# Optimization experiments

Hardware: AMD Instinct MI355X
Metric: run time of the kernel (lower is better)

The kernel has to match this reference:

```python
import jax, jax.numpy as jnp
import numpy as np


def setup_inputs() -> dict:
    key = jax.random.key(0)
    ks = jax.random.split(key, 5)
    B, S, D, H, DK = 2, 2048, 1024, 16, 64
    scale = 1.0 / np.sqrt(D)
    return {
        "x": jax.random.normal(ks[0], (B, S, D), dtype=jnp.float32),
        "Wq": jax.random.normal(ks[1], (H, D, DK), dtype=jnp.float32) * scale,
        "Wk": jax.random.normal(ks[2], (H, D, DK), dtype=jnp.float32) * scale,
        "Wv": jax.random.normal(ks[3], (H, D, DK), dtype=jnp.float32) * scale,
        "Wo": jax.random.normal(ks[4], (D, D), dtype=jnp.float32) * scale,
    }


def reference(x, Wq, Wk, Wv, Wo):
    # x: (B, S, D); Wq/Wk/Wv: (H, D, d_k); Wo: (D, D) torch-Linear convention (y = c @ Wo.T)
    B, S, D = x.shape
    H, _, dk = Wq.shape
    Q = jnp.einsum('bsd,hdk->bhsk', x, Wq)  # (B,H,S,dk)
    K = jnp.einsum('bsd,hdk->bhsk', x, Wk)
    V = jnp.einsum('bsd,hdk->bhsk', x, Wv)
    scores = jnp.einsum('bhqk,bhsk->bhqs', Q, K) / jnp.sqrt(jnp.float32(dk))  # (B,H,S,S)
    causal = jnp.tril(jnp.ones((S, S), dtype=bool))
    scores = jnp.where(causal[None, None, :, :], scores, -jnp.inf)
    weights = jax.nn.softmax(scores, axis=-1)
    out = jnp.einsum('bhqs,bhsk->bhqk', weights, V)  # (B,H,S,dk)
    concat = out.transpose(0, 2, 1, 3).reshape(B, S, H * dk)  # heads concatenated h-major
    return concat @ Wo.T
```

## Files before the change

### kernel.cpp

```cpp
#include <hip/hip_runtime.h>

typedef unsigned short u16;
typedef unsigned int u32;
typedef __bf16 bf16x8 __attribute__((ext_vector_type(8)));
typedef float f32x4 __attribute__((ext_vector_type(4)));
typedef u16 u16x8 __attribute__((ext_vector_type(8)));
typedef u16 u16x4 __attribute__((ext_vector_type(4)));
typedef u32 u32x4 __attribute__((ext_vector_type(4)));

#define NH 16
#define DKK 64
#define SQ 2048
#define DD 1024

#define AS1 __attribute__((address_space(1)))
#define AS3 __attribute__((address_space(3)))

#define QSCALE 0.1803368925f

#define WAIT4 do { asm volatile("s_waitcnt vmcnt(4)" ::: "memory"); \
                   __builtin_amdgcn_sched_barrier(0); } while (0)
#define WAIT3 do { asm volatile("s_waitcnt vmcnt(3)" ::: "memory"); \
                   __builtin_amdgcn_sched_barrier(0); } while (0)
#define WAIT0 do { asm volatile("s_waitcnt vmcnt(0)" ::: "memory"); \
                   __builtin_amdgcn_sched_barrier(0); } while (0)
#define LWAIT0 do { asm volatile("s_waitcnt lgkmcnt(0)" ::: "memory"); \
                    __builtin_amdgcn_sched_barrier(0); } while (0)
#define BAR   __builtin_amdgcn_s_barrier()

__device__ inline u16 f2bf(float f) {
  union { float f; u32 u; } v; v.f = f;
  u32 u = v.u;
  u += 0x7FFFu + ((u >> 16) & 1u);
  return (u16)(u >> 16);
}

__device__ __forceinline__ u32 cvtpk(float lo, float hi) {
  u32 r;
  asm("v_cvt_pk_bf16_f32 %0, %1, %2" : "=v"(r) : "v"(lo), "v"(hi));
  return r;
}

__device__ inline u16x8 cvt8(const float* p) {
  float4 a = *(const float4*)p;
  float4 b = *(const float4*)(p + 4);
  u16x8 v;
  v[0] = f2bf(a.x); v[1] = f2bf(a.y); v[2] = f2bf(a.z); v[3] = f2bf(a.w);
  v[4] = f2bf(b.x); v[5] = f2bf(b.y); v[6] = f2bf(b.z); v[7] = f2bf(b.w);
  return v;
}

__device__ __forceinline__ void gload16(const u16* g, u16* l) {
  __builtin_amdgcn_global_load_lds((const AS1 u32*)(const void*)g,
                                   (AS3 u32*)(void*)l, 16, 0, 0);
}

__global__ __launch_bounds__(256) void prep_kernel(const float* __restrict__ x,
                                                   u16* __restrict__ xb,
                                                   const float* __restrict__ Wo,
                                                   u16* __restrict__ Wob,
                                                   const float* __restrict__ Wq,
                                                   const float* __restrict__ Wk,
                                                   const float* __restrict__ Wv,
                                                   u16* __restrict__ WT) {
  __shared__ u16 sm[64][72];
  int bid = blockIdx.x;
  int tid = threadIdx.x;
  if (bid < 2560) {
    const float* src; u16* dst; size_t base;
    if (bid < 2048) { src = x;  dst = xb;  base = (size_t)bid * 2048; }
    else            { src = Wo; dst = Wob; base = (size_t)(bid - 2048) * 2048; }
    size_t off = base + (size_t)tid * 8;
    *(u16x8*)&dst[off] = cvt8(&src[off]);
    return;
  }
  int wid = bid - 2560;
  int t = wid >> 8;
  int rem = wid & 255;
  int h = rem >> 4;
  int d0 = (rem & 15) * 64;
  const float* src = (t == 0) ? Wq : (t == 1) ? Wk : Wv;
  for (int j = 0; j < 2; ++j) {
    int idx = tid + j * 256;
    int r = idx >> 3;
    int c0 = (idx & 7) * 8;
    *(u16x8*)&sm[r][c0] = cvt8(&src[(h * DD + d0 + r) * DKK + c0]);
  }
  __syncthreads();
  for (int j = 0; j < 2; ++j) {
    int idx = tid + j * 256;
    int r2 = idx >> 3;
    int c0 = (idx & 7) * 8;
    u16x8 vv;
    for (int i = 0; i < 8; ++i) vv[i] = sm[c0 + i][r2];
    int n = t * 1024 + h * 64 + r2;
    *(u16x8*)&WT[n * DD + d0 + c0] = vv;
  }
}

__global__ __launch_bounds__(256) void gemm128(const u16* __restrict__ A,
                                               const u16* __restrict__ Bm,
                                               u16* __restrict__ o0,
                                               u16* __restrict__ o1,
                                               u16* __restrict__ o2) {
  __shared__ u16 As[2][128 * 32];
  __shared__ u16 Bs[2][128 * 32];
  const int K = 1024;
  int m0 = blockIdx.x * 128;
  int n0 = blockIdx.y * 128;
  int tid = threadIdx.x;
  int w = tid >> 6, l = tid & 63;
  int lg = l >> 4, lr = l & 15;
  int wr = w >> 1, wc = w & 1;

  int srow = w * 32 + (l >> 2);
  int sg = (l & 3) ^ ((l >> 3) & 3);
  const u16* gA = A + (size_t)(m0 + srow) * K + sg * 8;
  const u16* gB = Bm + (size_t)(n0 + srow) * K + sg * 8;
  int gsw = (lr >> 1) & 3;

  #define GSTAGE(buf, k0)                              \
    do {                                               \
      gload16(gA + (k0), &As[buf][w * 1024]);          \
      gload16(gA + (k0) + 16 * K, &As[buf][w * 1024 + 512]); \
      gload16(gB + (k0), &Bs[buf][w * 1024]);          \
      gload16(gB + (k0) + 16 * K, &Bs[buf][w * 1024 + 512]); \
    } while (0)

  f32x4 acc[4][4] = {};
  GSTAGE(0, 0);
  for (int kt = 0; kt < 32; ++kt) {
    int buf = kt & 1;
    if (kt < 31) { GSTAGE(buf ^ 1, (kt + 1) * 32); WAIT4; }
    else         { WAIT0; }
    BAR;
    bf16x8 a[4], b[4];
    #pragma unroll
    for (int m = 0; m < 4; ++m)
      a[m] = *(const bf16x8*)&As[buf][(wr * 64 + m * 16 + lr) * 32 + ((lg ^ gsw) * 8)];
    #pragma unroll
    for (int n = 0; n < 4; ++n)
      b[n] = *(const bf16x8*)&Bs[buf][(wc * 64 + n * 16 + lr) * 32 + ((lg ^ gsw) * 8)];
    #pragma unroll
    for (int m = 0; m < 4; ++m)
      #pragma unroll
      for (int n = 0; n < 4; ++n)
        acc[m][n] = __builtin_amdgcn_mfma_f32_16x16x32_bf16(a[m], b[n], acc[m][n], 0, 0, 0);
    BAR;
  }
  #undef GSTAGE

  {
    int t = n0 >> 10;
    int h = (((n0 & 1023) + wc * 64) >> 6);
    int bq = m0 >> 11;
    int sbase = (m0 & 2047) + wr * 64 + lg * 4;
    if (t < 2) {
      float sc = (t == 0) ? QSCALE : 1.0f;
      u16* o = (t == 0) ? o0 : o1;
      u16* op = o + (size_t)(bq * NH + h) * SQ * DKK;
      #pragma unroll
      for (int m = 0; m < 4; ++m)
        #pragma unroll
        for (int n = 0; n < 4; ++n)
          #pragma unroll
          for (int rr = 0; rr < 4; ++rr)
            op[(size_t)(sbase + m * 16 + rr) * DKK + n * 16 + lr] = f2bf(acc[m][n][rr] * sc);
    } else {
      u16* op = o2 + (size_t)(bq * NH + h) * DKK * SQ;
      int Sb = (m0 & 2047) + wr * 64;
      #pragma unroll
      for (int m = 0; m < 4; ++m)
        #pragma unroll
        for (int n = 0; n < 4; ++n) {
          u16x4 vv;
          #pragma unroll
          for (int rr = 0; rr < 4; ++rr) vv[rr] = f2bf(acc[m][n][rr]);
          *(u16x4*)&op[(size_t)(n * 16 + lr) * SQ + Sb + (m >> 1) * 32 + lg * 8 + (m & 1) * 4] = vv;
        }
    }
  }
}

__global__ __launch_bounds__(256) void gemm_wo(const u16* __restrict__ A,
                                               const u16* __restrict__ Bm,
                                               float* __restrict__ of) {
  __shared__ u16 As[2][128 * 32];
  __shared__ u16 Bs[2][64 * 32];
  const int K = 1024;
  int m0 = blockIdx.x * 128;
  int n0 = blockIdx.y * 64;
  int tid = threadIdx.x;
  int w = tid >> 6, l = tid & 63;
  int lg = l >> 4, lr = l & 15;
  int wr = w >> 1, wc = w & 1;

  int sg = (l & 3) ^ ((l >> 3) & 3);
  const u16* gA = A + (size_t)(m0 + w * 32 + (l >> 2)) * K + sg * 8;
  const u16* gB = Bm + (size_t)(n0 + w * 16 + (l >> 2)) * K + sg * 8;
  int gsw = (lr >> 1) & 3;

  #define WSTAGE(buf, k0)                              \
    do {                                               \
      gload16(gA + (k0), &As[buf][w * 1024]);          \
      gload16(gA + (k0) + 16 * K, &As[buf][w * 1024 + 512]); \
      gload16(gB + (k0), &Bs[buf][w * 512]);           \
    } while (0)

  f32x4 acc[4][2] = {};
  WSTAGE(0, 0);
  for (int kt = 0; kt < 32; ++kt) {
    int buf = kt & 1;
    if (kt < 31) { WSTAGE(buf ^ 1, (kt + 1) * 32); WAIT3; }
    else         { WAIT0; }
    BAR;
    bf16x8 a[4], b[2];
    #pragma unroll
    for (int m = 0; m < 4; ++m)
      a[m] = *(const bf16x8*)&As[buf][(wr * 64 + m * 16 + lr) * 32 + ((lg ^ gsw) * 8)];
    #pragma unroll
    for (int n = 0; n < 2; ++n)
      b[n] = *(const bf16x8*)&Bs[buf][(wc * 32 + n * 16 + lr) * 32 + ((lg ^ gsw) * 8)];
    #pragma unroll
    for (int m = 0; m < 4; ++m)
      #pragma unroll
      for (int n = 0; n < 2; ++n)
        acc[m][n] = __builtin_amdgcn_mfma_f32_16x16x32_bf16(a[m], b[n], acc[m][n], 0, 0, 0);
    BAR;
  }
  #undef WSTAGE

  int mbase = m0 + wr * 64 + lg * 4;
  int nbase = n0 + wc * 32 + lr;
  #pragma unroll
  for (int m = 0; m < 4; ++m)
    #pragma unroll
    for (int n = 0; n < 2; ++n)
      #pragma unroll
      for (int rr = 0; rr < 4; ++rr)
        of[(size_t)(mbase + m * 16 + rr) * 1024 + nbase + n * 16] = acc[m][n][rr];
}

__global__ __launch_bounds__(256) void attn_kernel(const u16* __restrict__ Q,
                                                   const u16* __restrict__ Kg,
                                                   const u16* __restrict__ Vt,
                                                   u16* __restrict__ Cc) {
  __shared__ u16 Ks[2][64 * 64];
  __shared__ u16 Vs[2][64 * 64];
  int bh = blockIdx.x;
  int y = blockIdx.y;
  int a = y & 7, bsel = y >> 3;
  int s = (bsel == 0) ? 2 * a : (bsel == 1) ? 2 * a + 1
        : (bsel == 2) ? 30 - 2 * a : 31 - 2 * a;
  int tid = threadIdx.x;
  int w = tid >> 6, l = tid & 63;
  int lg = l >> 4, lr = l & 15;
  const u16* Qp = Q + (size_t)bh * SQ * DKK;
  const u16* Kp = Kg + (size_t)bh * SQ * DKK;
  const u16* Vp = Vt + (size_t)bh * DKK * SQ;
  int b = bh >> 4, h = bh & 15;

  int lrow8 = l >> 3;
  int swz = (l & 7) ^ lrow8;
  int r7 = lr & 7;
  const u16* kSrc0 = Kp + (size_t)(w * 16 + lrow8) * DKK + swz * 8;
  const u16* kSrc1 = Kp + (size_t)(w * 16 + 8 + lrow8) * DKK + swz * 8;
  const u16* vSrc0 = Vp + (size_t)(w * 16 + lrow8) * SQ + swz * 8;
  const u16* vSrc1 = Vp + (size_t)(w * 16 + 8 + lrow8) * SQ + swz * 8;

  #define STAGE(buf, j0)                                                  \
    do {                                                                  \
      gload16(kSrc0 + (size_t)(j0) * DKK, &Ks[buf][(w * 16) * 64]);       \
      gload16(kSrc1 + (size_t)(j0) * DKK, &Ks[buf][(w * 16 + 8) * 64]);   \
      gload16(vSrc0 + (j0), &Vs[buf][(w * 16) * 64]);                     \
      gload16(vSrc1 + (j0), &Vs[buf][(w * 16 + 8) * 64]);                 \
    } while (0)

  int qrow = s * 64 + w * 16 + lr;
  bf16x8 qf0 = *(const bf16x8*)&Qp[(size_t)qrow * DKK + lg * 8];
  bf16x8 qf1 = *(const bf16x8*)&Qp[(size_t)qrow * DKK + 32 + lg * 8];

  STAGE(0, 0);

  f32x4 o[4] = {};
  float lpart = 0.f, suPrev = 0.f;
  union { u16x8 u; bf16x8 v; } zz;
  #pragma unroll
  for (int i = 0; i < 8; ++i) zz.u[i] = 0;
  bf16x8 paPrev0 = zz.v, paPrev1 = zz.v;
  bf16x8 vPrev0[4], vPrev1[4];
  #pragma unroll
  for (int n = 0; n < 4; ++n) { vPrev0[n] = zz.v; vPrev1[n] = zz.v; }

  for (int jt = 0; jt <= s; ++jt) {
    int cur = jt & 1;
    if (jt < s) { STAGE(cur ^ 1, (jt + 1) * 64); WAIT4; }
    else        { WAIT0; }
    BAR;

    float p[16];
    __builtin_amdgcn_s_setprio(1);
    #pragma unroll
    for (int c = 0; c < 4; ++c) {
      int R = c * 16 + lr;
      const u16* kr = &Ks[cur][R * 64];
      bf16x8 k0 = *(const bf16x8*)&kr[(lg ^ r7) * 8];
      bf16x8 k1 = *(const bf16x8*)&kr[((4 + lg) ^ r7) * 8];
      f32x4 z = {};
      z = __builtin_amdgcn_mfma_f32_16x16x32_bf16(k0, qf0, z, 0, 0, 0);
      z = __builtin_amdgcn_mfma_f32_16x16x32_bf16(k1, qf1, z, 0, 0, 0);
      #pragma unroll
      for (int rr = 0; rr < 4; ++rr) p[c * 4 + rr] = z[rr];
    }
    #pragma unroll
    for (int n = 0; n < 4; ++n) {
      o[n] = __builtin_amdgcn_mfma_f32_16x16x32_bf16(paPrev0, vPrev0[n], o[n], 0, 0, 0);
      o[n] = __builtin_amdgcn_mfma_f32_16x16x32_bf16(paPrev1, vPrev1[n], o[n], 0, 0, 0);
    }
    __builtin_amdgcn_s_setprio(0);
    lpart += suPrev;
    #pragma unroll
    for (int n = 0; n < 4; ++n) {
      int R2 = n * 16 + lr;
      vPrev0[n] = *(const bf16x8*)&Vs[cur][R2 * 64 + ((lg ^ r7) * 8)];
      vPrev1[n] = *(const bf16x8*)&Vs[cur][R2 * 64 + (((4 + lg) ^ r7) * 8)];
    }
    if (jt == s) {
      int j0 = jt * 64;
      #pragma unroll
      for (int c = 0; c < 4; ++c)
        #pragma unroll
        for (int rr = 0; rr < 4; ++rr) {
          int kv = j0 + c * 16 + lg * 4 + rr;
          if (kv > qrow) p[c * 4 + rr] = -1e30f;
        }
    }
    float su = 0.f;
    #pragma unroll
    for (int i = 0; i < 16; ++i) { p[i] = exp2f(p[i]); su += p[i]; }
    suPrev = su;
    union { u32x4 w; bf16x8 v; } pk0, pk1;
    pk0.w[0] = cvtpk(p[0],  p[1]);
    pk0.w[1] = cvtpk(p[2],  p[3]);
    pk0.w[2] = cvtpk(p[4],  p[5]);
    pk0.w[3] = cvtpk(p[6],  p[7]);
    pk1.w[0] = cvtpk(p[8],  p[9]);
    pk1.w[1] = cvtpk(p[10], p[11]);
    pk1.w[2] = cvtpk(p[12], p[13]);
    pk1.w[3] = cvtpk(p[14], p[15]);
    paPrev0 = pk0.v;
    paPrev1 = pk1.v;
    LWAIT0;
    BAR;
  }

  #pragma unroll
  for (int n = 0; n < 4; ++n) {
    o[n] = __builtin_amdgcn_mfma_f32_16x16x32_bf16(paPrev0, vPrev0[n], o[n], 0, 0, 0);
    o[n] = __builtin_amdgcn_mfma_f32_16x16x32_bf16(paPrev1, vPrev1[n], o[n], 0, 0, 0);
  }
  lpart += suPrev;

  float lsum = lpart;
  lsum += __shfl_xor(lsum, 16, 64);
  lsum += __shfl_xor(lsum, 32, 64);
  float lrow[4];
  #pragma unroll
  for (int rr = 0; rr < 4; ++rr) lrow[rr] = __shfl(lsum, lg * 4 + rr, 64);
  int srow = s * 64 + w * 16 + lg * 4;
  #pragma unroll
  for (int n = 0; n < 4; ++n)
    #pragma unroll
    for (int rr = 0; rr < 4; ++rr) {
      float val = o[n][rr] / lrow[rr];
      Cc[((size_t)(b * SQ + srow + rr)) * DD + h * DKK + n * 16 + lr] = f2bf(val);
    }
  #undef STAGE
}

extern "C" void kernel_launch(void* const* d_in, const int* in_sizes, int n_in,
                              void* d_out, int out_size, void* d_ws, size_t ws_size,
                              hipStream_t stream) {
  (void)in_sizes; (void)n_in; (void)out_size; (void)ws_size;
  const float* x  = (const float*)d_in[0];
  const float* Wq = (const float*)d_in[1];
  const float* Wk = (const float*)d_in[2];
  const float* Wv = (const float*)d_in[3];
  const float* Wo = (const float*)d_in[4];
  float* out = (float*)d_out;
  u16* ws = (u16*)d_ws;
  u16* WT  = ws;
  u16* Qb  = WT + 3145728;
  u16* Kb  = Qb + 4194304;
  u16* Vb  = Kb + 4194304;
  u16* XC  = Vb + 4194304;
  u16* Wob = XC + 4194304;

  hipLaunchKernelGGL(prep_kernel, dim3(3328), dim3(256), 0, stream, x, XC, Wo, Wob, Wq, Wk, Wv, WT);
  hipLaunchKernelGGL(gemm128, dim3(32, 24), dim3(256), 0, stream, XC, WT, Qb, Kb, Vb);
  hipLaunchKernelGGL(attn_kernel, dim3(32, 32), dim3(256), 0, stream, Qb, Kb, Vb, XC);
  hipLaunchKernelGGL(gemm_wo, dim3(32, 16), dim3(256), 0, stream, XC, Wob, out);
}
```

Before: 106.7 us.

## Triple-buffer LDS staging in QKV GEMM and attention to drop a barrier

New measurement: 131.7 us. 1.23x slower.

```diff
diff --git a/kernel.cpp b/kernel.cpp
--- a/kernel.cpp
+++ b/kernel.cpp
@@ -103,8 +103,8 @@
                                                u16* __restrict__ o0,
                                                u16* __restrict__ o1,
                                                u16* __restrict__ o2) {
-  __shared__ u16 As[2][128 * 32];
-  __shared__ u16 Bs[2][128 * 32];
+  __shared__ u16 As[3][128 * 32];
+  __shared__ u16 Bs[3][128 * 32];
   const int K = 1024;
   int m0 = blockIdx.x * 128;
   int n0 = blockIdx.y * 128;
@@ -127,28 +127,34 @@
       gload16(gB + (k0) + 16 * K, &Bs[buf][w * 1024 + 512]); \
     } while (0)
 
+  #define GCOMP(BC)                                                            \
+    do {                                                                       \
+      bf16x8 a[4], b[4];                                                       \
+      _Pragma("unroll")                                                        \
+      for (int m = 0; m < 4; ++m)                                              \
+        a[m] = *(const bf16x8*)&As[BC][(wr * 64 + m * 16 + lr) * 32 + ((lg ^ gsw) * 8)]; \
+      _Pragma("unroll")                                                        \
+      for (int n = 0; n < 4; ++n)                                              \
+        b[n] = *(const bf16x8*)&Bs[BC][(wc * 64 + n * 16 + lr) * 32 + ((lg ^ gsw) * 8)]; \
+      _Pragma("unroll")                                                        \
+      for (int m = 0; m < 4; ++m)                                              \
+        _Pragma("unroll")                                                      \
+        for (int n = 0; n < 4; ++n)                                            \
+          acc[m][n] = __builtin_amdgcn_mfma_f32_16x16x32_bf16(a[m], b[n], acc[m][n], 0, 0, 0); \
+    } while (0)
+
   f32x4 acc[4][4] = {};
   GSTAGE(0, 0);
-  for (int kt = 0; kt < 32; ++kt) {
-    int buf = kt & 1;
-    if (kt < 31) { GSTAGE(buf ^ 1, (kt + 1) * 32); WAIT4; }
-    else         { WAIT0; }
-    BAR;
-    bf16x8 a[4], b[4];
-    #pragma unroll
-    for (int m = 0; m < 4; ++m)
-      a[m] = *(const bf16x8*)&As[buf][(wr * 64 + m * 16 + lr) * 32 + ((lg ^ gsw) * 8)];
-    #pragma unroll
-    for (int n = 0; n < 4; ++n)
-      b[n] = *(const bf16x8*)&Bs[buf][(wc * 64 + n * 16 + lr) * 32 + ((lg ^ gsw) * 8)];
-    #pragma unroll
-    for (int m = 0; m < 4; ++m)
-      #pragma unroll
-      for (int n = 0; n < 4; ++n)
-        acc[m][n] = __builtin_amdgcn_mfma_f32_16x16x32_bf16(a[m], b[n], acc[m][n], 0, 0, 0);
-    BAR;
-  }
+  GSTAGE(1, 32);
+  for (int kt = 0; kt < 30; kt += 3) {
+    WAIT4; BAR; GSTAGE(2, (kt + 2) * 32); GCOMP(0);
+    WAIT4; BAR; GSTAGE(0, (kt + 3) * 32); GCOMP(1);
+    WAIT4; BAR; GSTAGE(1, (kt + 4) * 32); GCOMP(2);
+  }
+  WAIT4; BAR; GCOMP(0);
+  WAIT0; BAR; GCOMP(1);
   #undef GSTAGE
+  #undef GCOMP
 
   {
     int t = n0 >> 10;
@@ -245,8 +251,8 @@
                                                    const u16* __restrict__ Kg,
                                                    const u16* __restrict__ Vt,
                                                    u16* __restrict__ Cc) {
-  __shared__ u16 Ks[2][64 * 64];
-  __shared__ u16 Vs[2][64 * 64];
+  __shared__ u16 Ks[3][64 * 64];
+  __shared__ u16 Vs[3][64 * 64];
   int bh = blockIdx.x;
   int y = blockIdx.y;
   int a = y & 7, bsel = y >> 3;
@@ -281,6 +287,7 @@
   bf16x8 qf1 = *(const bf16x8*)&Qp[(size_t)qrow * DKK + 32 + lg * 8];
 
   STAGE(0, 0);
+  if (s >= 1) STAGE(1, 64);
 
   f32x4 o[4] = {};
   float lpart = 0.f, suPrev = 0.f;
@@ -292,11 +299,14 @@
   #pragma unroll
   for (int n = 0; n < 4; ++n) { vPrev0[n] = zz.v; vPrev1[n] = zz.v; }
 
+  int cur = 0;
   for (int jt = 0; jt <= s; ++jt) {
-    int cur = jt & 1;
-    if (jt < s) { STAGE(cur ^ 1, (jt + 1) * 64); WAIT4; }
-    else        { WAIT0; }
+    if (jt < s) WAIT4; else WAIT0;
     BAR;
+    if (jt + 2 <= s) {
+      int bs = (cur == 0) ? 2 : cur - 1;
+      STAGE(bs, (jt + 2) * 64);
+    }
 
     float p[16];
     __builtin_amdgcn_s_setprio(1);
@@ -351,7 +361,7 @@
     paPrev0 = pk0.v;
     paPrev1 = pk1.v;
     LWAIT0;
-    BAR;
+    cur = (cur == 2) ? 0 : cur + 1;
   }
 
   #pragma unroll
```

## Split long causal attention rows across two blocks and combine partial sums

Applied to the files above, without the earlier changes.

Result: slower. 110.6 us (+3.7%).

```diff
diff --git a/kernel.cpp b/kernel.cpp
--- a/kernel.cpp
+++ b/kernel.cpp
@@ -28,11 +28,26 @@
                     __builtin_amdgcn_sched_barrier(0); } while (0)
 #define BAR   __builtin_amdgcn_s_barrier()
 
+__constant__ int TS[48]  = {15,31,31,30,14,13,28,11,  28,29,29,30,12,23,24,21,
+                            26,27,27,26,22,23,20,21,  24,25,25,18,16,19,19,22,
+                             6, 5, 4, 7,17,17,20,10,   0, 1, 2, 3,16,18, 8, 9};
+__constant__ int TT0[48] = { 0, 0,16, 0, 0, 0,15, 0,   0, 0,15,16, 0, 0,13, 0,
+                             0, 0,14,14, 0,12, 0,11,   0, 0,13, 0, 0, 0,10,12,
+                             0, 0, 0, 0, 0, 9,11, 0,   0, 0, 0, 0, 9,10, 0, 0};
+__constant__ int TNT[48] = {16,16,16,16,15,14,14,12,  15,15,15,15,13,12,12,11,
+                            14,14,14,13,12,12,11,11,  13,13,13,10, 9,10,10,11,
+                             7, 6, 5, 8, 9, 9,10,11,   1, 2, 3, 4, 8, 9, 9,10};
+
 __device__ inline u16 f2bf(float f) {
   union { float f; u32 u; } v; v.f = f;
   u32 u = v.u;
   u += 0x7FFFu + ((u >> 16) & 1u);
   return (u16)(u >> 16);
+}
+
+__device__ inline float bf2f(u16 x) {
+  union { u32 u; float f; } v; v.u = ((u32)x) << 16;
+  return v.f;
 }
 
 __device__ __forceinline__ u32 cvtpk(float lo, float hi) {
@@ -244,14 +259,17 @@
 __global__ __launch_bounds__(256) void attn_kernel(const u16* __restrict__ Q,
                                                    const u16* __restrict__ Kg,
                                                    const u16* __restrict__ Vt,
-                                                   u16* __restrict__ Cc) {
+                                                   u16* __restrict__ Cc,
+                                                   u16* __restrict__ oP,
+                                                   float* __restrict__ lP) {
   __shared__ u16 Ks[2][64 * 64];
   __shared__ u16 Vs[2][64 * 64];
   int bh = blockIdx.x;
   int y = blockIdx.y;
-  int a = y & 7, bsel = y >> 3;
-  int s = (bsel == 0) ? 2 * a : (bsel == 1) ? 2 * a + 1
-        : (bsel == 2) ? 30 - 2 * a : 31 - 2 * a;
+  int s = TS[y], t0 = TT0[y], nt = TNT[y];
+  int tend = t0 + nt - 1;
+  bool masked = (tend == s);
+  bool partial = (s >= 16);
   int tid = threadIdx.x;
   int w = tid >> 6, l = tid & 63;
   int lg = l >> 4, lr = l & 15;
@@ -280,7 +298,7 @@
   bf16x8 qf0 = *(const bf16x8*)&Qp[(size_t)qrow * DKK + lg * 8];
   bf16x8 qf1 = *(const bf16x8*)&Qp[(size_t)qrow * DKK + 32 + lg * 8];
 
-  STAGE(0, 0);
+  STAGE(0, t0 * 64);
 
   f32x4 o[4] = {};
   float lpart = 0.f, suPrev = 0.f;
@@ -292,10 +310,10 @@
   #pragma unroll
   for (int n = 0; n < 4; ++n) { vPrev0[n] = zz.v; vPrev1[n] = zz.v; }
 
-  for (int jt = 0; jt <= s; ++jt) {
-    int cur = jt & 1;
-    if (jt < s) { STAGE(cur ^ 1, (jt + 1) * 64); WAIT4; }
-    else        { WAIT0; }
+  for (int jt = t0; jt <= tend; ++jt) {
+    int cur = (jt - t0) & 1;
+    if (jt < tend) { STAGE(cur ^ 1, (jt + 1) * 64); WAIT4; }
+    else           { WAIT0; }
     BAR;
 
     float p[16];
@@ -325,7 +343,7 @@
       vPrev0[n] = *(const bf16x8*)&Vs[cur][R2 * 64 + ((lg ^ r7) * 8)];
       vPrev1[n] = *(const bf16x8*)&Vs[cur][R2 * 64 + (((4 + lg) ^ r7) * 8)];
     }
-    if (jt == s) {
+    if (masked && jt == s) {
       int j0 = jt * 64;
       #pragma unroll
       for (int c = 0; c < 4; ++c)
@@ -364,18 +382,58 @@
   float lsum = lpart;
   lsum += __shfl_xor(lsum, 16, 64);
   lsum += __shfl_xor(lsum, 32, 64);
-  float lrow[4];
+
+  if (!partial) {
+    float lrow[4];
+    #pragma unroll
+    for (int rr = 0; rr < 4; ++rr) lrow[rr] = __shfl(lsum, lg * 4 + rr, 64);
+    int srow = s * 64 + w * 16 + lg * 4;
+    #pragma unroll
+    for (int n = 0; n < 4; ++n)
+      #pragma unroll
+      for (int rr = 0; rr < 4; ++rr) {
+        float val = o[n][rr] / lrow[rr];
+        Cc[((size_t)(b * SQ + srow + rr)) * DD + h * DKK + n * 16 + lr] = f2bf(val);
+      }
+  } else {
+    int half = (t0 != 0) ? 1 : 0;
+    size_t cb = ((size_t)(bh * 16 + (s - 16)) * 2 + half);
+    u16* op = oP + cb * 4096;
+    #pragma unroll
+    for (int n = 0; n < 4; ++n)
+      #pragma unroll
+      for (int rr = 0; rr < 4; ++rr)
+        op[(w * 16 + lg * 4 + rr) * 64 + n * 16 + lr] = f2bf(o[n][rr]);
+    if (lg == 0) lP[cb * 64 + w * 16 + lr] = lsum;
+  }
+  #undef STAGE
+}
+
+__global__ __launch_bounds__(256) void combine_kernel(const u16* __restrict__ oP,
+                                                      const float* __restrict__ lP,
+                                                      u16* __restrict__ Cc) {
+  int bh = blockIdx.x;
+  int ss = blockIdx.y;
+  int tid = threadIdx.x;
+  int row = tid >> 2;
+  int c0 = (tid & 3) * 16;
+  size_t base = (size_t)(bh * 16 + ss) * 2;
+  float inv = 1.0f / (lP[base * 64 + row] + lP[(base + 1) * 64 + row]);
+  const u16* pA = oP + base * 4096 + row * 64 + c0;
+  const u16* pB = oP + (base + 1) * 4096 + row * 64 + c0;
+  int s = ss + 16;
+  int b = bh >> 4, h = bh & 15;
+  u16* dst = Cc + ((size_t)(b * SQ + s * 64 + row)) * DD + h * DKK + c0;
+  u16x8 a0 = *(const u16x8*)pA, a1 = *(const u16x8*)(pA + 8);
+  u16x8 b0 = *(const u16x8*)pB, b1 = *(const u16x8*)(pB + 8);
+  u16x8 r0, r1;
   #pragma unroll
-  for (int rr = 0; rr < 4; ++rr) lrow[rr] = __shfl(lsum, lg * 4 + rr, 64);
-  int srow = s * 64 + w * 16 + lg * 4;
-  #pragma unroll
-  for (int n = 0; n < 4; ++n)
-    #pragma unroll
-    for (int rr = 0; rr < 4; ++rr) {
-      float val = o[n][rr] / lrow[rr];
-      Cc[((size_t)(b * SQ + srow + rr)) * DD + h * DKK + n * 16 + lr] = f2bf(val);
-    }
-  #undef STAGE
+  for (int i = 0; i < 8; ++i) {
+    r0[i] = f2bf((bf2f(a0[i]) + bf2f(b0[i])) * inv);
+    r1[i] = f2bf((bf2f(a1[i]) + bf2f(b1[i])) * inv);
+  }
+  *(u16x8*)dst = r0;
+  *(u16x8*)(dst + 8) = r1;
 }
 
 extern "C" void kernel_launch(void* const* d_in, const int* in_sizes, int n_in,
@@ -395,9 +453,12 @@
   u16* Vb  = Kb + 4194304;
   u16* XC  = Vb + 4194304;
   u16* Wob = XC + 4194304;
+  u16* oP  = Wob + 1048576;
+  float* lP = (float*)(oP + 4194304);
 
   hipLaunchKernelGGL(prep_kernel, dim3(3328), dim3(256), 0, stream, x, XC, Wo, Wob, Wq, Wk, Wv, WT);
   hipLaunchKernelGGL(gemm128, dim3(32, 24), dim3(256), 0, stream, XC, WT, Qb, Kb, Vb);
-  hipLaunchKernelGGL(attn_kernel, dim3(32, 32), dim3(256), 0, stream, Qb, Kb, Vb, XC);
+  hipLaunchKernelGGL(attn_kernel, dim3(32, 48), dim3(256), 0, stream, Qb, Kb, Vb, XC, oP, lP);
+  hipLaunchKernelGGL(combine_kernel, dim3(32, 16), dim3(256), 0, stream, oP, lP, XC);
   hipLaunchKernelGGL(gemm_wo, dim3(32, 16), dim3(256), 0, stream, XC, Wob, out);
 }
```
